# Performance work log

Hardware: AMD Instinct MI355X
Metric: run time of the kernel (lower is better)

Reference implementation:

```python
import jax, jax.numpy as jnp
import numpy as np

N_NODES = 100000
N_EDGES = 3200000  # avg degree 32
IN_DIM = 116       # fixed by GCNConv(116, hidden)
HIDDEN = 256


def setup_inputs() -> dict:
    key = jax.random.key(0)
    k1, k2, k3 = jax.random.split(key, 3)
    x = jax.random.normal(k1, (N_NODES, IN_DIM), dtype=jnp.float32)
    edge_index = jax.random.randint(k2, (2, N_EDGES), 0, N_NODES, dtype=jnp.int32)
    # GCNConv linear weight (stored here as [in, out]) and bias
    W = jax.random.normal(k3, (IN_DIM, HIDDEN), dtype=jnp.float32) * (1.0 / np.sqrt(IN_DIM))
    b = jnp.zeros((HIDDEN,), dtype=jnp.float32)
    return {"x": x, "edge_index": edge_index, "W": W, "b": b}


def reference(x, edge_index, W, b):
    # GCNConv: out = D^{-1/2} (A + I) D^{-1/2} (x W) + b ; then ReLU
    n = x.shape[0]
    loops = jnp.arange(n, dtype=edge_index.dtype)
    src = jnp.concatenate([edge_index[0], loops])  # [E + N]
    dst = jnp.concatenate([edge_index[1], loops])
    # degree of target nodes after self-loops (edge weight 1)
    deg = jax.ops.segment_sum(jnp.ones_like(src, dtype=x.dtype), dst, num_segments=n)
    dinv = jnp.where(deg > 0, jax.lax.rsqrt(deg), 0.0)
    norm = dinv[src] * dinv[dst]                   # [E + N]
    h = x @ W                                      # [N, H] project first (IN->H)
    msgs = h[src] * norm[:, None]                  # gather + scale
    agg = jax.ops.segment_sum(msgs, dst, num_segments=n)  # scatter-add
    return jax.nn.relu(agg + b)
```

## Files before the change

### kernel.cpp

```cpp
#include <hip/hip_runtime.h>


static constexpr int IN_DIM = 116;
static constexpr int PDIM   = 128;
static constexpr int HID    = 256;
static constexpr int BSH    = 8;
static constexpr int BNODES = 256;
static constexpr int NBPAD  = 512;
static constexpr int CHUNK  = 4096;
static constexpr int ECAP   = 9216;

typedef __attribute__((ext_vector_type(8))) short short8;
typedef __attribute__((ext_vector_type(4))) float f32x4;

__device__ __forceinline__ float bf_lo(uint u) { return __uint_as_float(u << 16); }
__device__ __forceinline__ float bf_hi(uint u) { return __uint_as_float(u & 0xffff0000u); }
__device__ __forceinline__ uint bf_pack(float a, float b) {
  uint ua = __float_as_uint(a); ua = (ua + 0x7fffu + ((ua >> 16) & 1u)) >> 16;
  uint ub = __float_as_uint(b); ub = (ub + 0x7fffu + ((ub >> 16) & 1u)) >> 16;
  return ua | (ub << 16);
}

__global__ __launch_bounds__(256) void k_bucket_hist(const int* __restrict__ dst, int E,
                                                     int* __restrict__ bcnt) {
  __shared__ int h[NBPAD];
  int tid = threadIdx.x;
  h[tid] = 0; h[tid + 256] = 0;
  __syncthreads();
  int stride = gridDim.x * 256;
  for (int e = blockIdx.x * 256 + tid; e < E; e += stride)
    atomicAdd(&h[dst[e] >> BSH], 1);
  __syncthreads();
  if (h[tid])       atomicAdd(&bcnt[tid], h[tid]);
  if (h[tid + 256]) atomicAdd(&bcnt[tid + 256], h[tid + 256]);
}

__global__ __launch_bounds__(256) void k_scan_b(const int* __restrict__ bcnt,
                                                int* __restrict__ bbase,
                                                int* __restrict__ bcursor) {
  __shared__ int s2[256];
  int t = threadIdx.x;
  int a = bcnt[2 * t], b = bcnt[2 * t + 1];
  s2[t] = a + b;
  __syncthreads();
  for (int off = 1; off < 256; off <<= 1) {
    int v = (t >= off) ? s2[t - off] : 0;
    __syncthreads();
    s2[t] += v;
    __syncthreads();
  }
  int ex2 = s2[t] - (a + b);
  bbase[2 * t] = ex2;         bcursor[2 * t] = ex2;
  bbase[2 * t + 1] = ex2 + a; bcursor[2 * t + 1] = ex2 + a;
}

__global__ __launch_bounds__(256) void k_scatter(const int* __restrict__ src,
                                                 const int* __restrict__ dst, int E,
                                                 int* __restrict__ bcursor,
                                                 uint* __restrict__ pairs) {
  __shared__ int hist[NBPAD];
  __shared__ int base[NBPAD];
  __shared__ int goff[NBPAD];
  __shared__ int s2[256];
  __shared__ uint stage[CHUNK];
  __shared__ unsigned short bkt[CHUNK];
  int tid = threadIdx.x;
  int cbase = blockIdx.x * CHUNK;
  int cnt = E - cbase; if (cnt > CHUNK) cnt = CHUNK;
  hist[tid] = 0; hist[tid + 256] = 0;
  __syncthreads();

  int db[16]; int rk[16]; uint pk[16];
#pragma unroll
  for (int j = 0; j < 16; ++j) {
    int idx = cbase + j * 256 + tid;
    if (idx < E) {
      int d = dst[idx];
      int b = d >> BSH;
      db[j] = b;
      pk[j] = ((uint)(d & (BNODES - 1)) << 24) | (uint)src[idx];
      rk[j] = atomicAdd(&hist[b], 1);
    } else {
      db[j] = -1;
    }
  }
  __syncthreads();
  {
    int a = hist[2 * tid], b = hist[2 * tid + 1];
    s2[tid] = a + b;
    __syncthreads();
    for (int off = 1; off < 256; off <<= 1) {
      int v = (tid >= off) ? s2[tid - off] : 0;
      __syncthreads();
      s2[tid] += v;
      __syncthreads();
    }
    int ex2 = s2[tid] - (a + b);
    base[2 * tid] = ex2; base[2 * tid + 1] = ex2 + a;
  }
  __syncthreads();
#pragma unroll
  for (int j = 0; j < 16; ++j)
    if (db[j] >= 0) {
      int pos = base[db[j]] + rk[j];
      stage[pos] = pk[j];
      bkt[pos] = (unsigned short)db[j];
    }
  for (int b = tid; b < NBPAD; b += 256) {
    int c = hist[b];
    if (c > 0) goff[b] = atomicAdd(&bcursor[b], c);
  }
  __syncthreads();
  for (int i = tid; i < cnt; i += 256) {
    int b = bkt[i];
    pairs[goff[b] + (i - base[b])] = stage[i];
  }
}

__global__ __launch_bounds__(256) void k_sort(const uint* __restrict__ pairs,
                                              const int* __restrict__ bbase,
                                              const int* __restrict__ bcursor,
                                              int* __restrict__ row_start,
                                              float* __restrict__ dinv,
                                              int* __restrict__ csr, int n) {
  __shared__ int h[BNODES];
  __shared__ int sc[BNODES];
  __shared__ int cur[BNODES];
  __shared__ int stage[ECAP];
  int b = blockIdx.x, tid = threadIdx.x;
  h[tid] = 0;
  __syncthreads();
  int s = bbase[b], epos = bcursor[b];
  for (int e = s + tid; e < epos; e += 256)
    atomicAdd(&h[pairs[e] >> 24], 1);
  __syncthreads();
  int len = h[tid];
  sc[tid] = len;
  __syncthreads();
  for (int off = 1; off < 256; off <<= 1) {
    int t = (tid >= off) ? sc[tid - off] : 0;
    __syncthreads();
    sc[tid] += t;
    __syncthreads();
  }
  int ex = sc[tid] - len;
  cur[tid] = ex;
  int v = (b << BSH) + tid;
  if (v < n) {
    row_start[v] = s + ex;
    dinv[v] = rsqrtf((float)(len + 1));
  }
  __syncthreads();
  for (int e = s + tid; e < epos; e += 256) {
    uint p = pairs[e];
    int pos = atomicAdd(&cur[p >> 24], 1);
    if (pos < ECAP) stage[pos] = (int)(p & 0xFFFFFFu);
  }
  __syncthreads();
  int cnt = epos - s; if (cnt > ECAP) cnt = ECAP;
  for (int i = tid; i < cnt; i += 256) csr[s + i] = stage[i];
}

__global__ __launch_bounds__(256) void k_scale(const float* __restrict__ x,
                                               const float* __restrict__ dinv,
                                               uint* __restrict__ xs, int n) {
  int gid = blockIdx.x * blockDim.x + threadIdx.x;
  int i = gid >> 4, q = gid & 15;
  if (i >= n) return;
  float dv = dinv[i];
  int c0 = q * 8;
  float c[8];
  if (c0 + 8 <= IN_DIM) {
    float4 v0 = *reinterpret_cast<const float4*>(x + (size_t)i * IN_DIM + c0);
    float4 v1 = *reinterpret_cast<const float4*>(x + (size_t)i * IN_DIM + c0 + 4);
    c[0] = v0.x; c[1] = v0.y; c[2] = v0.z; c[3] = v0.w;
    c[4] = v1.x; c[5] = v1.y; c[6] = v1.z; c[7] = v1.w;
  } else if (c0 < IN_DIM) {
    float4 v0 = *reinterpret_cast<const float4*>(x + (size_t)i * IN_DIM + c0);
    c[0] = v0.x; c[1] = v0.y; c[2] = v0.z; c[3] = v0.w;
    c[4] = c[5] = c[6] = c[7] = 0.f;
  } else {
    c[0] = c[1] = c[2] = c[3] = c[4] = c[5] = c[6] = c[7] = 0.f;
  }
#pragma unroll
  for (int j = 0; j < 8; ++j) c[j] *= dv;
  uint4 o;
  o.x = bf_pack(c[0], c[1]); o.y = bf_pack(c[2], c[3]);
  o.z = bf_pack(c[4], c[5]); o.w = bf_pack(c[6], c[7]);
  *reinterpret_cast<uint4*>(xs + (size_t)i * (PDIM / 2) + q * 4) = o;
}

__global__ __launch_bounds__(256) void k_agg3(const int* __restrict__ csr,
                                              const int* __restrict__ row_start,
                                              const float* __restrict__ dinv,
                                              const uint* __restrict__ xs,
                                              uint* __restrict__ aggb, int n, int E) {
  int gw = (blockIdx.x * 256 + threadIdx.x) >> 6;
  int lane = threadIdx.x & 63;
  if (gw >= n) return;
  int v = gw;
  int s0 = row_start[v];
  int s1 = (v + 1 < n) ? row_start[v + 1] : E;
  uint u = xs[(size_t)v * 64 + lane];
  float ax = bf_lo(u), ay = bf_hi(u);
  int e = s0;
  for (; e + 16 <= s1; e += 16) {
    int sj[16]; uint r[16];
#pragma unroll
    for (int j = 0; j < 16; ++j) sj[j] = csr[e + j];
#pragma unroll
    for (int j = 0; j < 16; ++j) r[j] = xs[(size_t)sj[j] * 64 + lane];
#pragma unroll
    for (int j = 0; j < 16; ++j) { ax += bf_lo(r[j]); ay += bf_hi(r[j]); }
  }
  for (; e + 4 <= s1; e += 4) {
    int sj[4]; uint r[4];
#pragma unroll
    for (int j = 0; j < 4; ++j) sj[j] = csr[e + j];
#pragma unroll
    for (int j = 0; j < 4; ++j) r[j] = xs[(size_t)sj[j] * 64 + lane];
#pragma unroll
    for (int j = 0; j < 4; ++j) { ax += bf_lo(r[j]); ay += bf_hi(r[j]); }
  }
  for (; e < s1; ++e) {
    uint r = xs[(size_t)csr[e] * 64 + lane];
    ax += bf_lo(r); ay += bf_hi(r);
  }
  float dv = dinv[v];
  aggb[(size_t)v * 64 + lane] = bf_pack(ax * dv, ay * dv);
}

__global__ __launch_bounds__(256) void k_prepw(const float* __restrict__ W,
                                               uint4* __restrict__ wfrag) {
  int t = blockIdx.x * 256 + threadIdx.x;
  int nc = t >> 8, ks = (t >> 6) & 3, l = t & 63;
  int kb = ks * 32 + (l >> 4) * 8;
  int c = nc * 16 + (l & 15);
  uint u[4];
#pragma unroll
  for (int p = 0; p < 4; ++p) {
    int k0 = kb + 2 * p, k1 = kb + 2 * p + 1;
    float f0 = (k0 < IN_DIM) ? W[(size_t)k0 * HID + c] : 0.f;
    float f1 = (k1 < IN_DIM) ? W[(size_t)k1 * HID + c] : 0.f;
    u[p] = bf_pack(f0, f1);
  }
  wfrag[t] = make_uint4(u[0], u[1], u[2], u[3]);
}

__global__ __launch_bounds__(256) void k_gemm_mfma(const uint4* __restrict__ aggb,
                                                   const uint4* __restrict__ wfrag,
                                                   const float* __restrict__ bias,
                                                   float* __restrict__ out, int n) {
  __shared__ uint4 At[128 * 16];
  int tid = threadIdx.x;
  int r0 = blockIdx.x * 128;

#pragma unroll
  for (int i = 0; i < 8; ++i) {
    int g = i * 256 + tid;
    int row = g >> 4, c = g & 15;
    int rr = r0 + row; if (rr >= n) rr = n - 1;
    At[row * 16 + (c ^ (row & 7))] = aggb[(size_t)rr * 16 + c];
  }
  __syncthreads();

  int wave = tid >> 6, lane = tid & 63;
  int lrow = lane & 15, lg = lane >> 4;
  int m0 = wave * 32;

  short8 a[2][4];
#pragma unroll
  for (int mf = 0; mf < 2; ++mf) {
    int row = m0 + mf * 16 + lrow;
#pragma unroll
    for (int ks = 0; ks < 4; ++ks) {
      int c = (ks * 4 + lg) ^ (row & 7);
      a[mf][ks] = *reinterpret_cast<const short8*>(&At[row * 16 + c]);
    }
  }

  f32x4 acc[2][16];
#pragma unroll
  for (int mf = 0; mf < 2; ++mf)
#pragma unroll
    for (int nc = 0; nc < 16; ++nc)
      acc[mf][nc] = (f32x4){0.f, 0.f, 0.f, 0.f};

#pragma unroll
  for (int nc = 0; nc < 16; ++nc) {
#pragma unroll
    for (int ks = 0; ks < 4; ++ks) {
      short8 bfr = *reinterpret_cast<const short8*>(&wfrag[(nc * 4 + ks) * 64 + lane]);
      acc[0][nc] = __builtin_amdgcn_mfma_f32_16x16x32_bf16(a[0][ks], bfr, acc[0][nc], 0, 0, 0);
      acc[1][nc] = __builtin_amdgcn_mfma_f32_16x16x32_bf16(a[1][ks], bfr, acc[1][nc], 0, 0, 0);
    }
  }

#pragma unroll
  for (int nc = 0; nc < 16; ++nc) {
    int col = nc * 16 + lrow;
    float bv = bias[col];
#pragma unroll
    for (int mf = 0; mf < 2; ++mf) {
#pragma unroll
      for (int r = 0; r < 4; ++r) {
        int rr = r0 + m0 + mf * 16 + lg * 4 + r;
        if (rr < n)
          out[(size_t)rr * HID + col] = fmaxf(acc[mf][nc][r] + bv, 0.f);
      }
    }
  }
}

extern "C" void kernel_launch(void* const* d_in, const int* in_sizes, int n_in,
                              void* d_out, int out_size, void* d_ws, size_t ws_size,
                              hipStream_t stream) {
  const float* x  = (const float*)d_in[0];
  const int*   ei = (const int*)d_in[1];
  const float* W  = (const float*)d_in[2];
  const float* bi = (const float*)d_in[3];
  float* out = (float*)d_out;

  int n = in_sizes[0] / IN_DIM;
  int E = in_sizes[1] / 2;
  const int* src = ei;
  const int* dst = ei + E;
  int NB = (n + BNODES - 1) >> BSH;

  char* p = (char*)d_ws;
  auto alloc = [&](size_t bytes) {
    char* r = p;
    p += (bytes + 255) & ~(size_t)255;
    return r;
  };
  int*   bcnt      = (int*)alloc(NBPAD * 4);
  int*   bbase     = (int*)alloc(NBPAD * 4);
  int*   bcursor   = (int*)alloc(NBPAD * 4);
  int*   row_start = (int*)alloc((size_t)n * 4);
  float* dinv      = (float*)alloc((size_t)n * 4);
  uint*  pairs     = (uint*)alloc((size_t)E * 4);
  int*   csr       = (int*)alloc((size_t)E * 4);
  uint*  xs        = (uint*)alloc((size_t)n * (PDIM / 2) * 4);
  uint*  aggb      = (uint*)alloc((size_t)n * (PDIM / 2) * 4);
  uint4* wfrag     = (uint4*)alloc(4096 * 16);

  (void)hipMemsetAsync(bcnt, 0, NBPAD * 4, stream);

  int nchunks = (E + CHUNK - 1) / CHUNK;
  hipLaunchKernelGGL(k_bucket_hist, dim3(nchunks), dim3(256), 0, stream, dst, E, bcnt);
  hipLaunchKernelGGL(k_scan_b, dim3(1), dim3(256), 0, stream, bcnt, bbase, bcursor);
  hipLaunchKernelGGL(k_scatter, dim3(nchunks), dim3(256), 0, stream, src, dst, E, bcursor, pairs);
  hipLaunchKernelGGL(k_sort, dim3(NB), dim3(256), 0, stream,
                     pairs, bbase, bcursor, row_start, dinv, csr, n);
  hipLaunchKernelGGL(k_scale, dim3((n * 16 + 255) / 256), dim3(256), 0, stream, x, dinv, xs, n);
  hipLaunchKernelGGL(k_prepw, dim3(16), dim3(256), 0, stream, W, wfrag);
  hipLaunchKernelGGL(k_agg3, dim3((n * 64 + 255) / 256), dim3(256), 0, stream,
                     csr, row_start, dinv, xs, aggb, n, E);
  hipLaunchKernelGGL(k_gemm_mfma, dim3((n + 127) / 128), dim3(256), 0, stream,
                     (const uint4*)aggb, wfrag, bi, out, n);
}
```

Measured before the change: 390.1 us.

## Add nontemporal hints and load GEMM A fragments directly from global

Marks streaming index loads (dst, src, csr) and the aggregated-feature store as nontemporal, so they are less likely to evict the gathered feature rows from cache. The GEMM kernel no longer stages its A tile through swizzled shared memory: each lane loads its bf16 fragment straight from global memory, which also removes the block barrier. Accumulators are now per output column chunk and written out immediately, which lowers register pressure. The cost is less coalesced global reads for A and possible loss of cache reuse on the aggb output.

Measured after the change: 373.4 us. -4.3%, faster.

```diff
diff --git a/kernel.cpp b/kernel.cpp
--- a/kernel.cpp
+++ b/kernel.cpp
@@ -29,7 +29,7 @@
   __syncthreads();
   int stride = gridDim.x * 256;
   for (int e = blockIdx.x * 256 + tid; e < E; e += stride)
-    atomicAdd(&h[dst[e] >> BSH], 1);
+    atomicAdd(&h[__builtin_nontemporal_load(&dst[e]) >> BSH], 1);
   __syncthreads();
   if (h[tid])       atomicAdd(&bcnt[tid], h[tid]);
   if (h[tid + 256]) atomicAdd(&bcnt[tid + 256], h[tid + 256]);
@@ -75,10 +75,10 @@
   for (int j = 0; j < 16; ++j) {
     int idx = cbase + j * 256 + tid;
     if (idx < E) {
-      int d = dst[idx];
+      int d = __builtin_nontemporal_load(&dst[idx]);
       int b = d >> BSH;
       db[j] = b;
-      pk[j] = ((uint)(d & (BNODES - 1)) << 24) | (uint)src[idx];
+      pk[j] = ((uint)(d & (BNODES - 1)) << 24) | (uint)__builtin_nontemporal_load(&src[idx]);
       rk[j] = atomicAdd(&hist[b], 1);
     } else {
       db[j] = -1;
@@ -207,7 +207,7 @@
   for (; e + 16 <= s1; e += 16) {
     int sj[16]; uint r[16];
 #pragma unroll
-    for (int j = 0; j < 16; ++j) sj[j] = csr[e + j];
+    for (int j = 0; j < 16; ++j) sj[j] = __builtin_nontemporal_load(&csr[e + j]);
 #pragma unroll
     for (int j = 0; j < 16; ++j) r[j] = xs[(size_t)sj[j] * 64 + lane];
 #pragma unroll
@@ -216,7 +216,7 @@
   for (; e + 4 <= s1; e += 4) {
     int sj[4]; uint r[4];
 #pragma unroll
-    for (int j = 0; j < 4; ++j) sj[j] = csr[e + j];
+    for (int j = 0; j < 4; ++j) sj[j] = __builtin_nontemporal_load(&csr[e + j]);
 #pragma unroll
     for (int j = 0; j < 4; ++j) r[j] = xs[(size_t)sj[j] * 64 + lane];
 #pragma unroll
@@ -227,7 +227,7 @@
     ax += bf_lo(r); ay += bf_hi(r);
   }
   float dv = dinv[v];
-  aggb[(size_t)v * 64 + lane] = bf_pack(ax * dv, ay * dv);
+  __builtin_nontemporal_store(bf_pack(ax * dv, ay * dv), &aggb[(size_t)v * 64 + lane]);
 }
 
 __global__ __launch_bounds__(256) void k_prepw(const float* __restrict__ W,
@@ -251,63 +251,40 @@
                                                    const uint4* __restrict__ wfrag,
                                                    const float* __restrict__ bias,
                                                    float* __restrict__ out, int n) {
-  __shared__ uint4 At[128 * 16];
   int tid = threadIdx.x;
-  int r0 = blockIdx.x * 128;
-
-#pragma unroll
-  for (int i = 0; i < 8; ++i) {
-    int g = i * 256 + tid;
-    int row = g >> 4, c = g & 15;
-    int rr = r0 + row; if (rr >= n) rr = n - 1;
-    At[row * 16 + (c ^ (row & 7))] = aggb[(size_t)rr * 16 + c];
-  }
-  __syncthreads();
-
   int wave = tid >> 6, lane = tid & 63;
   int lrow = lane & 15, lg = lane >> 4;
-  int m0 = wave * 32;
+  int r0 = blockIdx.x * 128 + wave * 32;
 
   short8 a[2][4];
 #pragma unroll
   for (int mf = 0; mf < 2; ++mf) {
-    int row = m0 + mf * 16 + lrow;
+    int rr = r0 + mf * 16 + lrow; if (rr >= n) rr = n - 1;
 #pragma unroll
     for (int ks = 0; ks < 4; ++ks) {
-      int c = (ks * 4 + lg) ^ (row & 7);
-      a[mf][ks] = *reinterpret_cast<const short8*>(&At[row * 16 + c]);
-    }
-  }
-
-  f32x4 acc[2][16];
-#pragma unroll
-  for (int mf = 0; mf < 2; ++mf)
-#pragma unroll
-    for (int nc = 0; nc < 16; ++nc)
-      acc[mf][nc] = (f32x4){0.f, 0.f, 0.f, 0.f};
+      uint4 t = aggb[(size_t)rr * 16 + ks * 4 + lg];
+      a[mf][ks] = *reinterpret_cast<const short8*>(&t);
+    }
+  }
 
 #pragma unroll
   for (int nc = 0; nc < 16; ++nc) {
+    f32x4 acc0 = (f32x4){0.f, 0.f, 0.f, 0.f};
+    f32x4 acc1 = (f32x4){0.f, 0.f, 0.f, 0.f};
 #pragma unroll
     for (int ks = 0; ks < 4; ++ks) {
       short8 bfr = *reinterpret_cast<const short8*>(&wfrag[(nc * 4 + ks) * 64 + lane]);
-      acc[0][nc] = __builtin_amdgcn_mfma_f32_16x16x32_bf16(a[0][ks], bfr, acc[0][nc], 0, 0, 0);
-      acc[1][nc] = __builtin_amdgcn_mfma_f32_16x16x32_bf16(a[1][ks], bfr, acc[1][nc], 0, 0, 0);
-    }
-  }
-
-#pragma unroll
-  for (int nc = 0; nc < 16; ++nc) {
+      acc0 = __builtin_amdgcn_mfma_f32_16x16x32_bf16(a[0][ks], bfr, acc0, 0, 0, 0);
+      acc1 = __builtin_amdgcn_mfma_f32_16x16x32_bf16(a[1][ks], bfr, acc1, 0, 0, 0);
+    }
     int col = nc * 16 + lrow;
     float bv = bias[col];
 #pragma unroll
-    for (int mf = 0; mf < 2; ++mf) {
-#pragma unroll
-      for (int r = 0; r < 4; ++r) {
-        int rr = r0 + m0 + mf * 16 + lg * 4 + r;
-        if (rr < n)
-          out[(size_t)rr * HID + col] = fmaxf(acc[mf][nc][r] + bv, 0.f);
-      }
+    for (int r = 0; r < 4; ++r) {
+      int rr0 = r0 + lg * 4 + r;
+      int rr1 = r0 + 16 + lg * 4 + r;
+      if (rr0 < n) out[(size_t)rr0 * HID + col] = fmaxf(acc0[r] + bv, 0.f);
+      if (rr1 < n) out[(size_t)rr1 * HID + col] = fmaxf(acc1[r] + bv, 0.f);
     }
   }
 }
```
